# Kernel tuning notes

Measured on AMD Instinct MI355X. Metric: run time of the kernel, lower is better.

## Reference

```python
import jax, jax.numpy as jnp
import numpy as np

N_NODES = 50000
N_EDGES = 800000
IN_CH = 128
HIDDEN = 64
OUT_CH = 32
N_REL = 8
N_GRAPHS = 64
NEG_SLOPE = 0.2  # RGATConv default leaky_relu slope


def setup_inputs() -> dict:
    key = jax.random.key(0)
    ks = jax.random.split(key, 20)
    s = 0.05
    inp = {
        "x": jax.random.normal(ks[0], (N_NODES, IN_CH), dtype=jnp.float32),
        "edge_index": jax.random.randint(ks[1], (2, N_EDGES), 0, N_NODES, dtype=jnp.int64),
        "edge_type": jax.random.randint(ks[2], (N_EDGES,), 0, N_REL, dtype=jnp.int64),
        "batch": jnp.sort(jax.random.randint(ks[3], (N_NODES,), 0, N_GRAPHS, dtype=jnp.int64)),
        # encoder Linear(in, hidden)
        "enc_W": jax.random.normal(ks[4], (IN_CH, HIDDEN), dtype=jnp.float32) * s,
        "enc_b": jnp.zeros((HIDDEN,), dtype=jnp.float32),
        # RGAT layer 0 (hidden -> hidden), heads=1, dim=1
        "w0": jax.random.normal(ks[5], (N_REL, HIDDEN, HIDDEN), dtype=jnp.float32) * s,
        "q0": jax.random.normal(ks[6], (HIDDEN, 1), dtype=jnp.float32) * s,
        "k0": jax.random.normal(ks[7], (HIDDEN, 1), dtype=jnp.float32) * s,
        "b0": jnp.zeros((HIDDEN,), dtype=jnp.float32),
        # RGAT layer 1 (hidden -> hidden)
        "w1": jax.random.normal(ks[8], (N_REL, HIDDEN, HIDDEN), dtype=jnp.float32) * s,
        "q1": jax.random.normal(ks[9], (HIDDEN, 1), dtype=jnp.float32) * s,
        "k1": jax.random.normal(ks[10], (HIDDEN, 1), dtype=jnp.float32) * s,
        "b1": jnp.zeros((HIDDEN,), dtype=jnp.float32),
        # head: Linear(hidden, hidden) + ReLU, then clf Linear(hidden, out)
        "lin_W": jax.random.normal(ks[11], (HIDDEN, HIDDEN), dtype=jnp.float32) * s,
        "lin_b": jnp.zeros((HIDDEN,), dtype=jnp.float32),
        "clf_W": jax.random.normal(ks[12], (HIDDEN, OUT_CH), dtype=jnp.float32) * s,
        "clf_b": jnp.zeros((OUT_CH,), dtype=jnp.float32),
    }
    return inp


def rgat_layer(h, src, dst, etype, w, q, k, b):
    # per-relation transform of all nodes: [R, N, out]
    h_all = jnp.einsum('ni,rio->rno', h, w)
    hi = h_all[etype, dst]          # [E, out] transformed target feats
    hj = h_all[etype, src]          # [E, out] transformed source feats
    # additive self-attention (heads=1, dim=1), across-relation softmax
    alpha = jax.nn.leaky_relu((hi @ q + hj @ k)[:, 0], NEG_SLOPE)  # [E]
    m = jax.ops.segment_max(alpha, dst, num_segments=N_NODES)
    e = jnp.exp(alpha - m[dst])
    ssum = jax.ops.segment_sum(e, dst, num_segments=N_NODES)
    a = e / jnp.maximum(ssum[dst], 1e-16)
    out = jax.ops.segment_sum(a[:, None] * hj, dst, num_segments=N_NODES)
    return out + b


def reference(x, edge_index, edge_type, batch,
              enc_W, enc_b, w0, q0, k0, b0, w1, q1, k1, b1,
              lin_W, lin_b, clf_W, clf_b):
    src, dst = edge_index[0], edge_index[1]
    h = x @ enc_W + enc_b                      # encoder
    h = rgat_layer(h, src, dst, edge_type, w0, q0, k0, b0)
    h = jax.nn.relu(h)                         # inter-layer relu (dropout=0)
    h = rgat_layer(h, src, dst, edge_type, w1, q1, k1, b1)
    pooled = jax.ops.segment_sum(h, batch, num_segments=N_GRAPHS)  # global_add_pool
    z = jax.nn.relu(pooled @ lin_W + lin_b)
    return z @ clf_W + clf_b                   # [N_GRAPHS, OUT_CH]
```

## Files before the change

### kernel.cpp

```cpp
#include <hip/hip_runtime.h>
#include <hip/hip_bf16.h>

#define NN 50000
#define NE 800000
#define INC 128
#define HID 64
#define OUTC 32
#define NREL 8
#define NG 64
#define SLOPE 0.2f
#define NB2 196
#define SCAP 6144
#define S_BLOCKS (NN / 16)

typedef unsigned int uint32;
typedef unsigned short ushort16;
typedef __attribute__((ext_vector_type(8))) short short8;
typedef __attribute__((ext_vector_type(4))) short short4v;
typedef __attribute__((ext_vector_type(4))) float float4v;
typedef __attribute__((ext_vector_type(4))) int int4v;

__device__ __forceinline__ float bf2f(ushort16 u) {
    union { uint32 i; float f; } v; v.i = ((uint32)u) << 16; return v.f;
}
__device__ __forceinline__ ushort16 f2bf(float f) {
    union { float f; uint32 i; } v; v.f = f;
    uint32 i = v.i;
    return (ushort16)((i + 0x7FFFu + ((i >> 16) & 1u)) >> 16);
}

__global__ __launch_bounds__(256) void enc_mfma(const float* __restrict__ x,
    const float* __restrict__ W, const float* __restrict__ bias,
    ushort16* __restrict__ hb)
{
    int tid = threadIdx.x, wv = tid >> 6, lane = tid & 63;
    int g = lane >> 4, lr = lane & 15;

    short8 bf[4][4];
    for (int t = 0; t < 4; ++t)
        for (int kc = 0; kc < 4; ++kc) {
            short8 v;
            #pragma unroll
            for (int j = 0; j < 8; ++j) {
                int k = kc * 32 + g * 8 + j;
                v[j] = (short)f2bf(W[k * HID + t * 16 + lr]);
            }
            bf[t][kc] = v;
        }

    __shared__ float lds[4][16 * 65];
    float* myl = lds[wv];

    for (int tile = blockIdx.x * 4 + wv; tile < NN / 16; tile += gridDim.x * 4) {
        int row0 = tile * 16;
        const float4v* xp = (const float4v*)(x + (size_t)(row0 + lr) * INC);
        short8 af[4];
        #pragma unroll
        for (int kc = 0; kc < 4; ++kc) {
            float4v u0 = xp[kc * 8 + g * 2];
            float4v u1 = xp[kc * 8 + g * 2 + 1];
            short8 v;
            v[0] = (short)f2bf(u0[0]); v[1] = (short)f2bf(u0[1]);
            v[2] = (short)f2bf(u0[2]); v[3] = (short)f2bf(u0[3]);
            v[4] = (short)f2bf(u1[0]); v[5] = (short)f2bf(u1[1]);
            v[6] = (short)f2bf(u1[2]); v[7] = (short)f2bf(u1[3]);
            af[kc] = v;
        }
        float4v acc[4];
        #pragma unroll
        for (int t = 0; t < 4; ++t) { float4v z = {0.f,0.f,0.f,0.f}; acc[t] = z; }
        #pragma unroll
        for (int t = 0; t < 4; ++t)
            #pragma unroll
            for (int kc = 0; kc < 4; ++kc)
                acc[t] = __builtin_amdgcn_mfma_f32_16x16x32_bf16(af[kc], bf[t][kc], acc[t], 0, 0, 0);

        #pragma unroll
        for (int t = 0; t < 4; ++t)
            #pragma unroll
            for (int i = 0; i < 4; ++i)
                myl[(4 * g + i) * 65 + t * 16 + lr] = acc[t][i];
        __asm volatile("s_waitcnt lgkmcnt(0)" ::: "memory");

        int row = lane >> 2, cg = lane & 3;
        const float* srcp = myl + row * 65 + cg * 16;
        uint32 p[8];
        #pragma unroll
        for (int j = 0; j < 8; ++j) {
            float v0 = srcp[2 * j]     + bias[cg * 16 + 2 * j];
            float v1 = srcp[2 * j + 1] + bias[cg * 16 + 2 * j + 1];
            p[j] = (uint32)f2bf(v0) | ((uint32)f2bf(v1) << 16);
        }
        int4v s0 = {(int)p[0], (int)p[1], (int)p[2], (int)p[3]};
        int4v s1 = {(int)p[4], (int)p[5], (int)p[6], (int)p[7]};
        int4v* op = (int4v*)(hb + (size_t)(row0 + row) * HID + cg * 16);
        op[0] = s0; op[1] = s1;
        __asm volatile("s_waitcnt lgkmcnt(0)" ::: "memory");
    }
}

__global__ __launch_bounds__(256) void sh_kernel(const ushort16* __restrict__ hb,
    const float* __restrict__ wqk, const float* __restrict__ w,
    float* __restrict__ sbuf, ushort16* __restrict__ hall)
{
    __shared__ float lds4[4][16 * 65];
    __shared__ float Ws[16 * 65];
    __shared__ short4v Hs[16][17];
    int tid = threadIdx.x;

    if (blockIdx.x < S_BLOCKS) {
        for (int i = tid; i < 16 * HID; i += 256) Ws[(i >> 6) * 65 + (i & 63)] = wqk[i];
        int n0 = blockIdx.x * 16;
        {
            int row = tid >> 4, ch = tid & 15;
            Hs[row][ch] = *(const short4v*)(hb + (size_t)(n0 + row) * HID + ch * 4);
        }
        __syncthreads();
        int j = tid & 15, nl = tid >> 4;
        short4v hreg[16];
        #pragma unroll
        for (int c = 0; c < 16; ++c) hreg[c] = Hs[nl][c];
        float acc = 0.f;
        #pragma unroll
        for (int c = 0; c < 16; ++c)
            #pragma unroll
            for (int u = 0; u < 4; ++u)
                acc += bf2f((ushort16)hreg[c][u]) * Ws[j * 65 + c * 4 + u];
        sbuf[(size_t)j * NN + n0 + nl] = acc;
        return;
    }

    int b = blockIdx.x - S_BLOCKS;
    int r = b >> 9, xb = b & 511;
    int wv = tid >> 6, lane = tid & 63;
    int g = lane >> 4, lr = lane & 15;
    const float* wr = w + (size_t)r * HID * HID;

    short8 bfr[4][2];
    for (int t = 0; t < 4; ++t)
        for (int kc = 0; kc < 2; ++kc) {
            short8 v;
            #pragma unroll
            for (int j = 0; j < 8; ++j) {
                int k = kc * 32 + g * 8 + j;
                v[j] = (short)f2bf(wr[k * HID + t * 16 + lr]);
            }
            bfr[t][kc] = v;
        }

    float* myl = lds4[wv];
    ushort16* outr = hall + (size_t)r * NN * HID;

    for (int tile = xb * 4 + wv; tile < NN / 16; tile += 512 * 4) {
        int row0 = tile * 16;
        const short8* ap = (const short8*)(hb + (size_t)(row0 + lr) * HID);
        short8 a0 = ap[g];
        short8 a1 = ap[4 + g];
        float4v acc[4];
        #pragma unroll
        for (int t = 0; t < 4; ++t) { float4v z = {0.f,0.f,0.f,0.f}; acc[t] = z; }
        #pragma unroll
        for (int t = 0; t < 4; ++t) {
            acc[t] = __builtin_amdgcn_mfma_f32_16x16x32_bf16(a0, bfr[t][0], acc[t], 0, 0, 0);
            acc[t] = __builtin_amdgcn_mfma_f32_16x16x32_bf16(a1, bfr[t][1], acc[t], 0, 0, 0);
        }
        #pragma unroll
        for (int t = 0; t < 4; ++t)
            #pragma unroll
            for (int i = 0; i < 4; ++i)
                myl[(4 * g + i) * 65 + t * 16 + lr] = acc[t][i];
        __asm volatile("s_waitcnt lgkmcnt(0)" ::: "memory");

        int row = lane >> 2, cg = lane & 3;
        const float* srcp = myl + row * 65 + cg * 16;
        uint32 p[8];
        #pragma unroll
        for (int j = 0; j < 8; ++j)
            p[j] = (uint32)f2bf(srcp[2 * j]) | ((uint32)f2bf(srcp[2 * j + 1]) << 16);
        int4v s0 = {(int)p[0], (int)p[1], (int)p[2], (int)p[3]};
        int4v s1 = {(int)p[4], (int)p[5], (int)p[6], (int)p[7]};
        int4v* op = (int4v*)(outr + (size_t)(row0 + row) * HID + cg * 16);
        op[0] = s0; op[1] = s1;
        __asm volatile("s_waitcnt lgkmcnt(0)" ::: "memory");
    }
}

__global__ __launch_bounds__(256) void prep_kernel(
    const float* __restrict__ w0, const float* __restrict__ q0, const float* __restrict__ k0,
    const float* __restrict__ w1, const float* __restrict__ q1, const float* __restrict__ k1,
    float* __restrict__ wqk0, float* __restrict__ wqk1,
    int* __restrict__ bucketHist)
{
    int b = blockIdx.x, t = threadIdx.x;
    if (b < 32) {
        const float* w  = (b < 16) ? w0 : w1;
        const float* qv = (b < 16) ? q0 : q1;
        const float* kv = (b < 16) ? k0 : k1;
        float* out = (b < 16) ? wqk0 : wqk1;
        int j = b & 15;
        int r = j & 7;
        const float* vv = (j < 8) ? qv : kv;
        if (t < 64) {
            const float* wr = w + ((size_t)r * HID + t) * HID;
            float acc = 0.f;
            for (int o = 0; o < HID; ++o) acc += wr[o] * vv[o];
            out[j * HID + t] = acc;
        }
    } else {
        if (t < NB2) bucketHist[t] = 0;
    }
}

__global__ __launch_bounds__(256) void histo196(const int* __restrict__ dst,
                                                int* __restrict__ bucketHist)
{
    __shared__ int lh[NB2];
    int t = threadIdx.x;
    for (int i = t; i < NB2; i += 256) lh[i] = 0;
    __syncthreads();
    int base = blockIdx.x * 2048;
    for (int i = t; i < 2048; i += 256) {
        int idx = base + i;
        if (idx < NE) atomicAdd(&lh[dst[idx] >> 8], 1);
    }
    __syncthreads();
    for (int i = t; i < NB2; i += 256) if (lh[i]) atomicAdd(&bucketHist[i], lh[i]);
}

__global__ __launch_bounds__(256) void scan196(const int* __restrict__ bucketHist,
    int* __restrict__ bucketBase, int* __restrict__ bucket_cur,
    float* __restrict__ pooled)
{
    __shared__ int ps[256];
    int t = threadIdx.x;
    int v = (t < NB2) ? bucketHist[t] : 0;
    ps[t] = v;
    __syncthreads();
    for (int off = 1; off < 256; off <<= 1) {
        int tv = (t >= off) ? ps[t - off] : 0;
        __syncthreads();
        ps[t] += tv;
        __syncthreads();
    }
    int excl = ps[t] - v;
    if (t < NB2) { bucketBase[t] = excl; bucket_cur[t] = excl; }
    if (t == 0) bucketBase[NB2] = NE;
    #pragma unroll
    for (int i = 0; i < (NG * HID) / 256; ++i) pooled[i * 256 + t] = 0.f;
}

__global__ __launch_bounds__(256) void binpass(const int* __restrict__ src,
    const int* __restrict__ dst, const int* __restrict__ et,
    int* __restrict__ bucket_cur, uint32* __restrict__ ebin)
{
    __shared__ int lh[NB2], lbase[NB2], lcur[NB2];
    int t = threadIdx.x;
    for (int i = t; i < NB2; i += 256) { lh[i] = 0; lcur[i] = 0; }
    __syncthreads();
    int base = blockIdx.x * 4096;
    uint32 rec[16]; int bkt[16];
    #pragma unroll
    for (int i = 0; i < 16; ++i) {
        int idx = base + i * 256 + t;
        bkt[i] = -1;
        if (idx < NE) {
            int s = src[idx], d = dst[idx], r = et[idx];
            rec[i] = (uint32)s | ((uint32)r << 16) | ((uint32)(d & 255) << 19);
            bkt[i] = d >> 8;
            atomicAdd(&lh[bkt[i]], 1);
        }
    }
    __syncthreads();
    for (int i = t; i < NB2; i += 256) if (lh[i]) lbase[i] = atomicAdd(&bucket_cur[i], lh[i]);
    __syncthreads();
    #pragma unroll
    for (int i = 0; i < 16; ++i) {
        if (bkt[i] >= 0) {
            int lpos = atomicAdd(&lcur[bkt[i]], 1);
            ebin[lbase[bkt[i]] + lpos] = rec[i];
        }
    }
}

__global__ __launch_bounds__(256) void sortpass(const uint32* __restrict__ ebin,
    const int* __restrict__ bucketBase, int* __restrict__ rowptr,
    uint32* __restrict__ edges_s)
{
    __shared__ uint32 stage[SCAP];
    __shared__ int cnt256[256], ps[256], cur[256];
    int b = blockIdx.x, t = threadIdx.x;
    int seg0 = bucketBase[b], seg1 = bucketBase[b + 1];
    int cnt = seg1 - seg0;
    cnt256[t] = 0;
    __syncthreads();
    for (int i = t; i < cnt; i += 256) {
        uint32 rec = ebin[seg0 + i];
        atomicAdd(&cnt256[(rec >> 19) & 255], 1);
    }
    __syncthreads();
    int v = cnt256[t];
    ps[t] = v;
    __syncthreads();
    for (int off = 1; off < 256; off <<= 1) {
        int tv = (t >= off) ? ps[t - off] : 0;
        __syncthreads();
        ps[t] += tv;
        __syncthreads();
    }
    int excl = ps[t] - v;
    int node = (b << 8) + t;
    if (node < NN) rowptr[node] = seg0 + excl;
    if (b == NB2 - 1 && t == 0) rowptr[NN] = NE;
    cur[t] = excl;
    __syncthreads();
    for (int i = t; i < cnt; i += 256) {
        uint32 rec = ebin[seg0 + i];
        int lpos = atomicAdd(&cur[(rec >> 19) & 255], 1);
        if (lpos < SCAP) stage[lpos] = rec;
        else edges_s[seg0 + lpos] = rec;
    }
    __syncthreads();
    int lim = cnt < SCAP ? cnt : SCAP;
    for (int i = t; i < lim; i += 256) edges_s[seg0 + i] = stage[i];
}

__global__ __launch_bounds__(256) void agg_kernel(const int* __restrict__ rowptr,
    const uint32* __restrict__ edges, const float* __restrict__ sbuf,
    const ushort16* __restrict__ hall, const float* __restrict__ bias,
    ushort16* __restrict__ out_bf, float* __restrict__ out_f32, int do_relu)
{
    int wv = threadIdx.x >> 6, lane = threadIdx.x & 63;
    int d = blockIdx.x * 4 + wv;
    if (d >= NN) return;
    int row0 = rowptr[d];
    int deg = rowptr[d + 1] - row0;
    int g = lane >> 3, cl = lane & 7;

    float myq = (lane < 8) ? sbuf[lane * NN + d] : 0.f;

    float acc[8];
    #pragma unroll
    for (int u = 0; u < 8; ++u) acc[u] = 0.f;
    float ssum = 0.f;

    for (int base = 0; base < deg; base += 16) {
        int j0 = base + g, j1 = j0 + 8;
        bool v0 = j0 < deg, v1 = j1 < deg;
        uint32 pk0 = v0 ? edges[row0 + j0] : 0u;
        uint32 pk1 = v1 ? edges[row0 + j1] : 0u;
        int s0 = (int)(pk0 & 0xFFFFu), r0 = (int)((pk0 >> 16) & 7u);
        int s1 = (int)(pk1 & 0xFFFFu), r1 = (int)((pk1 >> 16) & 7u);
        float sc0 = sbuf[(8 + r0) * NN + s0];
        float sc1 = sbuf[(8 + r1) * NN + s1];
        short8 hv0 = *(const short8*)(hall + ((size_t)r0 * NN + s0) * HID + cl * 8);
        short8 hv1 = *(const short8*)(hall + ((size_t)r1 * NN + s1) * HID + cl * 8);
        float a0 = __shfl(myq, r0) + sc0; a0 = (a0 > 0.f) ? a0 : SLOPE * a0;
        float a1 = __shfl(myq, r1) + sc1; a1 = (a1 > 0.f) ? a1 : SLOPE * a1;
        float ex0 = v0 ? __expf(a0) : 0.f;
        float ex1 = v1 ? __expf(a1) : 0.f;
        ssum += ex0 + ex1;
        #pragma unroll
        for (int u = 0; u < 8; ++u)
            acc[u] += ex0 * bf2f((ushort16)hv0[u]) + ex1 * bf2f((ushort16)hv1[u]);
    }

    #pragma unroll
    for (int o = 8; o < 64; o <<= 1) {
        ssum += __shfl_xor(ssum, o);
        #pragma unroll
        for (int u = 0; u < 8; ++u) acc[u] += __shfl_xor(acc[u], o);
    }

    if (lane < 8) {
        float inv = 1.f / fmaxf(ssum, 1e-16f);
        float o_[8];
        #pragma unroll
        for (int u = 0; u < 8; ++u) o_[u] = acc[u] * inv + bias[lane * 8 + u];
        if (do_relu) {
            uint32 p[4];
            #pragma unroll
            for (int u = 0; u < 4; ++u) {
                float v0 = fmaxf(o_[2 * u], 0.f);
                float v1 = fmaxf(o_[2 * u + 1], 0.f);
                p[u] = (uint32)f2bf(v0) | ((uint32)f2bf(v1) << 16);
            }
            int4v pk4 = {(int)p[0], (int)p[1], (int)p[2], (int)p[3]};
            *(int4v*)(out_bf + (size_t)d * HID + lane * 8) = pk4;
        } else {
            float4v v0 = {o_[0], o_[1], o_[2], o_[3]};
            float4v v1 = {o_[4], o_[5], o_[6], o_[7]};
            float4v* op = (float4v*)(out_f32 + (size_t)d * HID + lane * 8);
            op[0] = v0; op[1] = v1;
        }
    }
}

__global__ void pool_kernel(const float* __restrict__ h, const int* __restrict__ batch,
                            float* __restrict__ pooled)
{
    int t = blockIdx.x * 256 + threadIdx.x;
    int c = t & 63;
    int chunk = t >> 6;
    if (chunk >= NN / 16) return;
    int n0 = chunk * 16;
    float acc = 0.f;
    int cur = batch[n0];
    for (int n = n0; n < n0 + 16; ++n) {
        int b = batch[n];
        if (b != cur) { atomicAdd(&pooled[cur * HID + c], acc); acc = 0.f; cur = b; }
        acc += h[(size_t)n * HID + c];
    }
    atomicAdd(&pooled[cur * HID + c], acc);
}

__global__ __launch_bounds__(256) void head_kernel(const float* __restrict__ pooled,
    const float* __restrict__ linW, const float* __restrict__ linb,
    const float* __restrict__ clfW, const float* __restrict__ clfb,
    float* __restrict__ out)
{
    __shared__ float z[NG * HID];
    __shared__ float p[NG * HID];
    int tid = threadIdx.x;
    for (int i = tid; i < NG * HID; i += 256) p[i] = pooled[i];
    __syncthreads();
    for (int idx = tid; idx < NG * HID; idx += 256) {
        int g = idx >> 6, c = idx & 63;
        float acc = linb[c];
        for (int k = 0; k < HID; ++k) acc += p[g * HID + k] * linW[k * HID + c];
        z[idx] = fmaxf(acc, 0.f);
    }
    __syncthreads();
    for (int idx = tid; idx < NG * OUTC; idx += 256) {
        int g = idx >> 5, c = idx & 31;
        float acc = clfb[c];
        for (int k = 0; k < HID; ++k) acc += z[g * HID + k] * clfW[k * OUTC + c];
        out[idx] = acc;
    }
}

extern "C" void kernel_launch(void* const* d_in, const int* in_sizes, int n_in,
                              void* d_out, int out_size, void* d_ws, size_t ws_size,
                              hipStream_t stream)
{
    const float* x      = (const float*)d_in[0];
    const int*   eidx   = (const int*)d_in[1];
    const int*   etype  = (const int*)d_in[2];
    const int*   batch  = (const int*)d_in[3];
    const float* enc_W  = (const float*)d_in[4];
    const float* enc_b  = (const float*)d_in[5];
    const float* w0     = (const float*)d_in[6];
    const float* q0     = (const float*)d_in[7];
    const float* k0     = (const float*)d_in[8];
    const float* b0     = (const float*)d_in[9];
    const float* w1     = (const float*)d_in[10];
    const float* q1     = (const float*)d_in[11];
    const float* k1     = (const float*)d_in[12];
    const float* b1     = (const float*)d_in[13];
    const float* lin_W  = (const float*)d_in[14];
    const float* lin_b  = (const float*)d_in[15];
    const float* clf_W  = (const float*)d_in[16];
    const float* clf_b  = (const float*)d_in[17];

    const int* srcp = eidx;
    const int* dstp = eidx + NE;

    char* wsb = (char*)d_ws;
    ushort16* h_bf    = (ushort16*)wsb;                 wsb += (size_t)NN * HID * 2;
    ushort16* hall_bf = (ushort16*)wsb;                 wsb += (size_t)NREL * NN * HID * 2;
    float*    h_f     = (float*)wsb;                    wsb += (size_t)NN * HID * 4;
    float*    sbuf    = (float*)wsb;                    wsb += (size_t)16 * NN * 4;
    float*    wqk0    = (float*)wsb;                    wsb += 16 * HID * 4;
    float*    wqk1    = (float*)wsb;                    wsb += 16 * HID * 4;
    float*    pooled  = (float*)wsb;                    wsb += NG * HID * 4;
    int*      rowptr  = (int*)wsb;                      wsb += (size_t)(NN + 64) * 4;
    int*      bucketHist = (int*)wsb;                   wsb += 256 * 4;
    int*      bucketBase = (int*)wsb;                   wsb += 256 * 4;
    int*      bucket_cur = (int*)wsb;                   wsb += 256 * 4;
    uint32*   ebin    = (uint32*)wsb;                   wsb += (size_t)NE * 4;
    uint32*   edges_s = (uint32*)wsb;                   wsb += (size_t)(NE + 64) * 4;

    prep_kernel<<<33, 256, 0, stream>>>(w0, q0, k0, w1, q1, k1, wqk0, wqk1, bucketHist);

    histo196<<<(NE + 2047) / 2048, 256, 0, stream>>>(dstp, bucketHist);
    scan196<<<1, 256, 0, stream>>>(bucketHist, bucketBase, bucket_cur, pooled);
    binpass<<<(NE + 4095) / 4096, 256, 0, stream>>>(srcp, dstp, etype, bucket_cur, ebin);
    sortpass<<<NB2, 256, 0, stream>>>(ebin, bucketBase, rowptr, edges_s);

    enc_mfma<<<512, 256, 0, stream>>>(x, enc_W, enc_b, h_bf);

    const int SH_GRID = S_BLOCKS + 512 * NREL;

    sh_kernel<<<SH_GRID, 256, 0, stream>>>(h_bf, wqk0, w0, sbuf, hall_bf);
    agg_kernel<<<(NN + 3) / 4, 256, 0, stream>>>(rowptr, edges_s, sbuf, hall_bf, b0,
                                                 h_bf, (float*)nullptr, 1);

    sh_kernel<<<SH_GRID, 256, 0, stream>>>(h_bf, wqk1, w1, sbuf, hall_bf);
    agg_kernel<<<(NN + 3) / 4, 256, 0, stream>>>(rowptr, edges_s, sbuf, hall_bf, b1,
                                                 (ushort16*)nullptr, h_f, 0);

    pool_kernel<<<(NN / 16 * HID + 255) / 256, 256, 0, stream>>>(h_f, batch, pooled);
    head_kernel<<<1, 256, 0, stream>>>(pooled, lin_W, lin_b, clf_W, clf_b, (float*)d_out);
}
```

Baseline: 183.6 us.

## Fuse encoder with edge histogram and fold bucket scan into consumers

The encoder GEMM and the destination-bucket histogram now run as one launch with disjoint block ranges, so the two independent stages can overlap. The single-block scan kernel is removed: binpass and sortpass each recompute the 196-entry prefix sum in shared memory, and the zeroing of bucket_cur and pooled moves into prep_kernel. Two kernel launches and their serialization gaps go away, at the cost of a small amount of redundant scan work in every binpass and sortpass block.

```diff
diff --git a/kernel.cpp b/kernel.cpp
--- a/kernel.cpp
+++ b/kernel.cpp
@@ -12,6 +12,8 @@
 #define NB2 196
 #define SCAP 6144
 #define S_BLOCKS (NN / 16)
+#define ENC_BLOCKS 512
+#define HISTO_BLOCKS ((NE + 2047) / 2048)
 
 typedef unsigned int uint32;
 typedef unsigned short ushort16;
@@ -29,167 +31,12 @@
     return (ushort16)((i + 0x7FFFu + ((i >> 16) & 1u)) >> 16);
 }
 
-__global__ __launch_bounds__(256) void enc_mfma(const float* __restrict__ x,
-    const float* __restrict__ W, const float* __restrict__ bias,
-    ushort16* __restrict__ hb)
-{
-    int tid = threadIdx.x, wv = tid >> 6, lane = tid & 63;
-    int g = lane >> 4, lr = lane & 15;
-
-    short8 bf[4][4];
-    for (int t = 0; t < 4; ++t)
-        for (int kc = 0; kc < 4; ++kc) {
-            short8 v;
-            #pragma unroll
-            for (int j = 0; j < 8; ++j) {
-                int k = kc * 32 + g * 8 + j;
-                v[j] = (short)f2bf(W[k * HID + t * 16 + lr]);
-            }
-            bf[t][kc] = v;
-        }
-
-    __shared__ float lds[4][16 * 65];
-    float* myl = lds[wv];
-
-    for (int tile = blockIdx.x * 4 + wv; tile < NN / 16; tile += gridDim.x * 4) {
-        int row0 = tile * 16;
-        const float4v* xp = (const float4v*)(x + (size_t)(row0 + lr) * INC);
-        short8 af[4];
-        #pragma unroll
-        for (int kc = 0; kc < 4; ++kc) {
-            float4v u0 = xp[kc * 8 + g * 2];
-            float4v u1 = xp[kc * 8 + g * 2 + 1];
-            short8 v;
-            v[0] = (short)f2bf(u0[0]); v[1] = (short)f2bf(u0[1]);
-            v[2] = (short)f2bf(u0[2]); v[3] = (short)f2bf(u0[3]);
-            v[4] = (short)f2bf(u1[0]); v[5] = (short)f2bf(u1[1]);
-            v[6] = (short)f2bf(u1[2]); v[7] = (short)f2bf(u1[3]);
-            af[kc] = v;
-        }
-        float4v acc[4];
-        #pragma unroll
-        for (int t = 0; t < 4; ++t) { float4v z = {0.f,0.f,0.f,0.f}; acc[t] = z; }
-        #pragma unroll
-        for (int t = 0; t < 4; ++t)
-            #pragma unroll
-            for (int kc = 0; kc < 4; ++kc)
-                acc[t] = __builtin_amdgcn_mfma_f32_16x16x32_bf16(af[kc], bf[t][kc], acc[t], 0, 0, 0);
-
-        #pragma unroll
-        for (int t = 0; t < 4; ++t)
-            #pragma unroll
-            for (int i = 0; i < 4; ++i)
-                myl[(4 * g + i) * 65 + t * 16 + lr] = acc[t][i];
-        __asm volatile("s_waitcnt lgkmcnt(0)" ::: "memory");
-
-        int row = lane >> 2, cg = lane & 3;
-        const float* srcp = myl + row * 65 + cg * 16;
-        uint32 p[8];
-        #pragma unroll
-        for (int j = 0; j < 8; ++j) {
-            float v0 = srcp[2 * j]     + bias[cg * 16 + 2 * j];
-            float v1 = srcp[2 * j + 1] + bias[cg * 16 + 2 * j + 1];
-            p[j] = (uint32)f2bf(v0) | ((uint32)f2bf(v1) << 16);
-        }
-        int4v s0 = {(int)p[0], (int)p[1], (int)p[2], (int)p[3]};
-        int4v s1 = {(int)p[4], (int)p[5], (int)p[6], (int)p[7]};
-        int4v* op = (int4v*)(hb + (size_t)(row0 + row) * HID + cg * 16);
-        op[0] = s0; op[1] = s1;
-        __asm volatile("s_waitcnt lgkmcnt(0)" ::: "memory");
-    }
-}
-
-__global__ __launch_bounds__(256) void sh_kernel(const ushort16* __restrict__ hb,
-    const float* __restrict__ wqk, const float* __restrict__ w,
-    float* __restrict__ sbuf, ushort16* __restrict__ hall)
-{
-    __shared__ float lds4[4][16 * 65];
-    __shared__ float Ws[16 * 65];
-    __shared__ short4v Hs[16][17];
-    int tid = threadIdx.x;
-
-    if (blockIdx.x < S_BLOCKS) {
-        for (int i = tid; i < 16 * HID; i += 256) Ws[(i >> 6) * 65 + (i & 63)] = wqk[i];
-        int n0 = blockIdx.x * 16;
-        {
-            int row = tid >> 4, ch = tid & 15;
-            Hs[row][ch] = *(const short4v*)(hb + (size_t)(n0 + row) * HID + ch * 4);
-        }
-        __syncthreads();
-        int j = tid & 15, nl = tid >> 4;
-        short4v hreg[16];
-        #pragma unroll
-        for (int c = 0; c < 16; ++c) hreg[c] = Hs[nl][c];
-        float acc = 0.f;
-        #pragma unroll
-        for (int c = 0; c < 16; ++c)
-            #pragma unroll
-            for (int u = 0; u < 4; ++u)
-                acc += bf2f((ushort16)hreg[c][u]) * Ws[j * 65 + c * 4 + u];
-        sbuf[(size_t)j * NN + n0 + nl] = acc;
-        return;
-    }
-
-    int b = blockIdx.x - S_BLOCKS;
-    int r = b >> 9, xb = b & 511;
-    int wv = tid >> 6, lane = tid & 63;
-    int g = lane >> 4, lr = lane & 15;
-    const float* wr = w + (size_t)r * HID * HID;
-
-    short8 bfr[4][2];
-    for (int t = 0; t < 4; ++t)
-        for (int kc = 0; kc < 2; ++kc) {
-            short8 v;
-            #pragma unroll
-            for (int j = 0; j < 8; ++j) {
-                int k = kc * 32 + g * 8 + j;
-                v[j] = (short)f2bf(wr[k * HID + t * 16 + lr]);
-            }
-            bfr[t][kc] = v;
-        }
-
-    float* myl = lds4[wv];
-    ushort16* outr = hall + (size_t)r * NN * HID;
-
-    for (int tile = xb * 4 + wv; tile < NN / 16; tile += 512 * 4) {
-        int row0 = tile * 16;
-        const short8* ap = (const short8*)(hb + (size_t)(row0 + lr) * HID);
-        short8 a0 = ap[g];
-        short8 a1 = ap[4 + g];
-        float4v acc[4];
-        #pragma unroll
-        for (int t = 0; t < 4; ++t) { float4v z = {0.f,0.f,0.f,0.f}; acc[t] = z; }
-        #pragma unroll
-        for (int t = 0; t < 4; ++t) {
-            acc[t] = __builtin_amdgcn_mfma_f32_16x16x32_bf16(a0, bfr[t][0], acc[t], 0, 0, 0);
-            acc[t] = __builtin_amdgcn_mfma_f32_16x16x32_bf16(a1, bfr[t][1], acc[t], 0, 0, 0);
-        }
-        #pragma unroll
-        for (int t = 0; t < 4; ++t)
-            #pragma unroll
-            for (int i = 0; i < 4; ++i)
-                myl[(4 * g + i) * 65 + t * 16 + lr] = acc[t][i];
-        __asm volatile("s_waitcnt lgkmcnt(0)" ::: "memory");
-
-        int row = lane >> 2, cg = lane & 3;
-        const float* srcp = myl + row * 65 + cg * 16;
-        uint32 p[8];
-        #pragma unroll
-        for (int j = 0; j < 8; ++j)
-            p[j] = (uint32)f2bf(srcp[2 * j]) | ((uint32)f2bf(srcp[2 * j + 1]) << 16);
-        int4v s0 = {(int)p[0], (int)p[1], (int)p[2], (int)p[3]};
-        int4v s1 = {(int)p[4], (int)p[5], (int)p[6], (int)p[7]};
-        int4v* op = (int4v*)(outr + (size_t)(row0 + row) * HID + cg * 16);
-        op[0] = s0; op[1] = s1;
-        __asm volatile("s_waitcnt lgkmcnt(0)" ::: "memory");
-    }
-}
-
 __global__ __launch_bounds__(256) void prep_kernel(
     const float* __restrict__ w0, const float* __restrict__ q0, const float* __restrict__ k0,
     const float* __restrict__ w1, const float* __restrict__ q1, const float* __restrict__ k1,
     float* __restrict__ wqk0, float* __restrict__ wqk1,
-    int* __restrict__ bucketHist)
+    int* __restrict__ bucketHist, int* __restrict__ bucket_cur,
+    float* __restrict__ pooled)
 {
     int b = blockIdx.x, t = threadIdx.x;
     if (b < 32) {
@@ -207,32 +54,194 @@
             out[j * HID + t] = acc;
         }
     } else {
-        if (t < NB2) bucketHist[t] = 0;
-    }
-}
-
-__global__ __launch_bounds__(256) void histo196(const int* __restrict__ dst,
-                                                int* __restrict__ bucketHist)
-{
+        if (t < NB2) { bucketHist[t] = 0; bucket_cur[t] = 0; }
+        #pragma unroll
+        for (int i = 0; i < (NG * HID) / 256; ++i) pooled[i * 256 + t] = 0.f;
+    }
+}
+
+__global__ __launch_bounds__(256) void enchisto_kernel(const float* __restrict__ x,
+    const float* __restrict__ W, const float* __restrict__ bias,
+    ushort16* __restrict__ hb,
+    const int* __restrict__ dst, int* __restrict__ bucketHist)
+{
+    __shared__ float lds[4][16 * 65];
     __shared__ int lh[NB2];
+    int tid = threadIdx.x;
+
+    if (blockIdx.x >= ENC_BLOCKS) {
+        for (int i = tid; i < NB2; i += 256) lh[i] = 0;
+        __syncthreads();
+        int base = (blockIdx.x - ENC_BLOCKS) * 2048;
+        for (int i = tid; i < 2048; i += 256) {
+            int idx = base + i;
+            if (idx < NE) atomicAdd(&lh[dst[idx] >> 8], 1);
+        }
+        __syncthreads();
+        for (int i = tid; i < NB2; i += 256) if (lh[i]) atomicAdd(&bucketHist[i], lh[i]);
+        return;
+    }
+
+    int wv = tid >> 6, lane = tid & 63;
+    int g = lane >> 4, lr = lane & 15;
+
+    short8 bf[4][4];
+    for (int t = 0; t < 4; ++t)
+        for (int kc = 0; kc < 4; ++kc) {
+            short8 v;
+            #pragma unroll
+            for (int j = 0; j < 8; ++j) {
+                int k = kc * 32 + g * 8 + j;
+                v[j] = (short)f2bf(W[k * HID + t * 16 + lr]);
+            }
+            bf[t][kc] = v;
+        }
+
+    float* myl = lds[wv];
+
+    for (int tile = blockIdx.x * 4 + wv; tile < NN / 16; tile += ENC_BLOCKS * 4) {
+        int row0 = tile * 16;
+        const float4v* xp = (const float4v*)(x + (size_t)(row0 + lr) * INC);
+        short8 af[4];
+        #pragma unroll
+        for (int kc = 0; kc < 4; ++kc) {
+            float4v u0 = xp[kc * 8 + g * 2];
+            float4v u1 = xp[kc * 8 + g * 2 + 1];
+            short8 v;
+            v[0] = (short)f2bf(u0[0]); v[1] = (short)f2bf(u0[1]);
+            v[2] = (short)f2bf(u0[2]); v[3] = (short)f2bf(u0[3]);
+            v[4] = (short)f2bf(u1[0]); v[5] = (short)f2bf(u1[1]);
+            v[6] = (short)f2bf(u1[2]); v[7] = (short)f2bf(u1[3]);
+            af[kc] = v;
+        }
+        float4v acc[4];
+        #pragma unroll
+        for (int t = 0; t < 4; ++t) { float4v z = {0.f,0.f,0.f,0.f}; acc[t] = z; }
+        #pragma unroll
+        for (int t = 0; t < 4; ++t)
+            #pragma unroll
+            for (int kc = 0; kc < 4; ++kc)
+                acc[t] = __builtin_amdgcn_mfma_f32_16x16x32_bf16(af[kc], bf[t][kc], acc[t], 0, 0, 0);
+
+        #pragma unroll
+        for (int t = 0; t < 4; ++t)
+            #pragma unroll
+            for (int i = 0; i < 4; ++i)
+                myl[(4 * g + i) * 65 + t * 16 + lr] = acc[t][i];
+        __asm volatile("s_waitcnt lgkmcnt(0)" ::: "memory");
+
+        int row = lane >> 2, cg = lane & 3;
+        const float* srcp = myl + row * 65 + cg * 16;
+        uint32 p[8];
+        #pragma unroll
+        for (int j = 0; j < 8; ++j) {
+            float v0 = srcp[2 * j]     + bias[cg * 16 + 2 * j];
+            float v1 = srcp[2 * j + 1] + bias[cg * 16 + 2 * j + 1];
+            p[j] = (uint32)f2bf(v0) | ((uint32)f2bf(v1) << 16);
+        }
+        int4v s0 = {(int)p[0], (int)p[1], (int)p[2], (int)p[3]};
+        int4v s1 = {(int)p[4], (int)p[5], (int)p[6], (int)p[7]};
+        int4v* op = (int4v*)(hb + (size_t)(row0 + row) * HID + cg * 16);
+        op[0] = s0; op[1] = s1;
+        __asm volatile("s_waitcnt lgkmcnt(0)" ::: "memory");
+    }
+}
+
+__global__ __launch_bounds__(256) void sh_kernel(const ushort16* __restrict__ hb,
+    const float* __restrict__ wqk, const float* __restrict__ w,
+    float* __restrict__ sbuf, ushort16* __restrict__ hall)
+{
+    __shared__ float lds4[4][16 * 65];
+    __shared__ float Ws[16 * 65];
+    __shared__ short4v Hs[16][17];
+    int tid = threadIdx.x;
+
+    if (blockIdx.x < S_BLOCKS) {
+        for (int i = tid; i < 16 * HID; i += 256) Ws[(i >> 6) * 65 + (i & 63)] = wqk[i];
+        int n0 = blockIdx.x * 16;
+        {
+            int row = tid >> 4, ch = tid & 15;
+            Hs[row][ch] = *(const short4v*)(hb + (size_t)(n0 + row) * HID + ch * 4);
+        }
+        __syncthreads();
+        int j = tid & 15, nl = tid >> 4;
+        short4v hreg[16];
+        #pragma unroll
+        for (int c = 0; c < 16; ++c) hreg[c] = Hs[nl][c];
+        float acc = 0.f;
+        #pragma unroll
+        for (int c = 0; c < 16; ++c)
+            #pragma unroll
+            for (int u = 0; u < 4; ++u)
+                acc += bf2f((ushort16)hreg[c][u]) * Ws[j * 65 + c * 4 + u];
+        sbuf[(size_t)j * NN + n0 + nl] = acc;
+        return;
+    }
+
+    int b = blockIdx.x - S_BLOCKS;
+    int r = b >> 9, xb = b & 511;
+    int wv = tid >> 6, lane = tid & 63;
+    int g = lane >> 4, lr = lane & 15;
+    const float* wr = w + (size_t)r * HID * HID;
+
+    short8 bfr[4][2];
+    for (int t = 0; t < 4; ++t)
+        for (int kc = 0; kc < 2; ++kc) {
+            short8 v;
+            #pragma unroll
+            for (int j = 0; j < 8; ++j) {
+                int k = kc * 32 + g * 8 + j;
+                v[j] = (short)f2bf(wr[k * HID + t * 16 + lr]);
+            }
+            bfr[t][kc] = v;
+        }
+
+    float* myl = lds4[wv];
+    ushort16* outr = hall + (size_t)r * NN * HID;
+
+    for (int tile = xb * 4 + wv; tile < NN / 16; tile += 512 * 4) {
+        int row0 = tile * 16;
+        const short8* ap = (const short8*)(hb + (size_t)(row0 + lr) * HID);
+        short8 a0 = ap[g];
+        short8 a1 = ap[4 + g];
+        float4v acc[4];
+        #pragma unroll
+        for (int t = 0; t < 4; ++t) { float4v z = {0.f,0.f,0.f,0.f}; acc[t] = z; }
+        #pragma unroll
+        for (int t = 0; t < 4; ++t) {
+            acc[t] = __builtin_amdgcn_mfma_f32_16x16x32_bf16(a0, bfr[t][0], acc[t], 0, 0, 0);
+            acc[t] = __builtin_amdgcn_mfma_f32_16x16x32_bf16(a1, bfr[t][1], acc[t], 0, 0, 0);
+        }
+        #pragma unroll
+        for (int t = 0; t < 4; ++t)
+            #pragma unroll
+            for (int i = 0; i < 4; ++i)
+                myl[(4 * g + i) * 65 + t * 16 + lr] = acc[t][i];
+        __asm volatile("s_waitcnt lgkmcnt(0)" ::: "memory");
+
+        int row = lane >> 2, cg = lane & 3;
+        const float* srcp = myl + row * 65 + cg * 16;
+        uint32 p[8];
+        #pragma unroll
+        for (int j = 0; j < 8; ++j)
+            p[j] = (uint32)f2bf(srcp[2 * j]) | ((uint32)f2bf(srcp[2 * j + 1]) << 16);
+        int4v s0 = {(int)p[0], (int)p[1], (int)p[2], (int)p[3]};
+        int4v s1 = {(int)p[4], (int)p[5], (int)p[6], (int)p[7]};
+        int4v* op = (int4v*)(outr + (size_t)(row0 + row) * HID + cg * 16);
+        op[0] = s0; op[1] = s1;
+        __asm volatile("s_waitcnt lgkmcnt(0)" ::: "memory");
+    }
+}
+
+__global__ __launch_bounds__(256) void binpass(const int* __restrict__ src,
+    const int* __restrict__ dst, const int* __restrict__ et,
+    const int* __restrict__ bucketHist,
+    int* __restrict__ bucket_cur, uint32* __restrict__ ebin)
+{
+    __shared__ int ps[256], baseSh[NB2];
+    __shared__ int lh[NB2], lbase[NB2], lcur[NB2];
     int t = threadIdx.x;
-    for (int i = t; i < NB2; i += 256) lh[i] = 0;
-    __syncthreads();
-    int base = blockIdx.x * 2048;
-    for (int i = t; i < 2048; i += 256) {
-        int idx = base + i;
-        if (idx < NE) atomicAdd(&lh[dst[idx] >> 8], 1);
-    }
-    __syncthreads();
-    for (int i = t; i < NB2; i += 256) if (lh[i]) atomicAdd(&bucketHist[i], lh[i]);
-}
-
-__global__ __launch_bounds__(256) void scan196(const int* __restrict__ bucketHist,
-    int* __restrict__ bucketBase, int* __restrict__ bucket_cur,
-    float* __restrict__ pooled)
-{
-    __shared__ int ps[256];
-    int t = threadIdx.x;
+
     int v = (t < NB2) ? bucketHist[t] : 0;
     ps[t] = v;
     __syncthreads();
@@ -242,21 +251,11 @@
         ps[t] += tv;
         __syncthreads();
     }
-    int excl = ps[t] - v;
-    if (t < NB2) { bucketBase[t] = excl; bucket_cur[t] = excl; }
-    if (t == 0) bucketBase[NB2] = NE;
-    #pragma unroll
-    for (int i = 0; i < (NG * HID) / 256; ++i) pooled[i * 256 + t] = 0.f;
-}
-
-__global__ __launch_bounds__(256) void binpass(const int* __restrict__ src,
-    const int* __restrict__ dst, const int* __restrict__ et,
-    int* __restrict__ bucket_cur, uint32* __restrict__ ebin)
-{
-    __shared__ int lh[NB2], lbase[NB2], lcur[NB2];
-    int t = threadIdx.x;
+    if (t < NB2) baseSh[t] = ps[t] - v;
+
     for (int i = t; i < NB2; i += 256) { lh[i] = 0; lcur[i] = 0; }
     __syncthreads();
+
     int base = blockIdx.x * 4096;
     uint32 rec[16]; int bkt[16];
     #pragma unroll
@@ -271,7 +270,8 @@
         }
     }
     __syncthreads();
-    for (int i = t; i < NB2; i += 256) if (lh[i]) lbase[i] = atomicAdd(&bucket_cur[i], lh[i]);
+    for (int i = t; i < NB2; i += 256)
+        if (lh[i]) lbase[i] = baseSh[i] + atomicAdd(&bucket_cur[i], lh[i]);
     __syncthreads();
     #pragma unroll
     for (int i = 0; i < 16; ++i) {
@@ -283,14 +283,28 @@
 }
 
 __global__ __launch_bounds__(256) void sortpass(const uint32* __restrict__ ebin,
-    const int* __restrict__ bucketBase, int* __restrict__ rowptr,
+    const int* __restrict__ bucketHist, int* __restrict__ rowptr,
     uint32* __restrict__ edges_s)
 {
     __shared__ uint32 stage[SCAP];
     __shared__ int cnt256[256], ps[256], cur[256];
+    __shared__ int segSh[2];
     int b = blockIdx.x, t = threadIdx.x;
-    int seg0 = bucketBase[b], seg1 = bucketBase[b + 1];
+
+    int v = (t < NB2) ? bucketHist[t] : 0;
+    ps[t] = v;
+    __syncthreads();
+    for (int off = 1; off < 256; off <<= 1) {
+        int tv = (t >= off) ? ps[t - off] : 0;
+        __syncthreads();
+        ps[t] += tv;
+        __syncthreads();
+    }
+    if (t == b) { segSh[0] = ps[t] - v; segSh[1] = ps[t]; }
+    __syncthreads();
+    int seg0 = segSh[0], seg1 = segSh[1];
     int cnt = seg1 - seg0;
+
     cnt256[t] = 0;
     __syncthreads();
     for (int i = t; i < cnt; i += 256) {
@@ -298,8 +312,8 @@
         atomicAdd(&cnt256[(rec >> 19) & 255], 1);
     }
     __syncthreads();
-    int v = cnt256[t];
-    ps[t] = v;
+    int v2 = cnt256[t];
+    ps[t] = v2;
     __syncthreads();
     for (int off = 1; off < 256; off <<= 1) {
         int tv = (t >= off) ? ps[t - off] : 0;
@@ -307,7 +321,7 @@
         ps[t] += tv;
         __syncthreads();
     }
-    int excl = ps[t] - v;
+    int excl = ps[t] - v2;
     int node = (b << 8) + t;
     if (node < NN) rowptr[node] = seg0 + excl;
     if (b == NB2 - 1 && t == 0) rowptr[NN] = NE;
@@ -474,19 +488,19 @@
     float*    pooled  = (float*)wsb;                    wsb += NG * HID * 4;
     int*      rowptr  = (int*)wsb;                      wsb += (size_t)(NN + 64) * 4;
     int*      bucketHist = (int*)wsb;                   wsb += 256 * 4;
-    int*      bucketBase = (int*)wsb;                   wsb += 256 * 4;
     int*      bucket_cur = (int*)wsb;                   wsb += 256 * 4;
     uint32*   ebin    = (uint32*)wsb;                   wsb += (size_t)NE * 4;
     uint32*   edges_s = (uint32*)wsb;                   wsb += (size_t)(NE + 64) * 4;
 
-    prep_kernel<<<33, 256, 0, stream>>>(w0, q0, k0, w1, q1, k1, wqk0, wqk1, bucketHist);
-
-    histo196<<<(NE + 2047) / 2048, 256, 0, stream>>>(dstp, bucketHist);
-    scan196<<<1, 256, 0, stream>>>(bucketHist, bucketBase, bucket_cur, pooled);
-    binpass<<<(NE + 4095) / 4096, 256, 0, stream>>>(srcp, dstp, etype, bucket_cur, ebin);
-    sortpass<<<NB2, 256, 0, stream>>>(ebin, bucketBase, rowptr, edges_s);
-
-    enc_mfma<<<512, 256, 0, stream>>>(x, enc_W, enc_b, h_bf);
+    prep_kernel<<<33, 256, 0, stream>>>(w0, q0, k0, w1, q1, k1, wqk0, wqk1,
+                                        bucketHist, bucket_cur, pooled);
+
+    enchisto_kernel<<<ENC_BLOCKS + HISTO_BLOCKS, 256, 0, stream>>>(
+        x, enc_W, enc_b, h_bf, dstp, bucketHist);
+
+    binpass<<<(NE + 4095) / 4096, 256, 0, stream>>>(srcp, dstp, etype,
+                                                    bucketHist, bucket_cur, ebin);
+    sortpass<<<NB2, 256, 0, stream>>>(ebin, bucketHist, rowptr, edges_s);
 
     const int SH_GRID = S_BLOCKS + 512 * NREL;
 
```

After: 178.6 us. 2.7% less time.
